# Kernel tuning notes

Hardware: AMD Instinct MI355X
Metric: run time of the kernel (lower is better)

Reference implementation:

```python
import jax, jax.numpy as jnp
import numpy as np

_SAMPLING_EPS = 1e-5
NEG_INF = jnp.float32(-jnp.inf)


def setup_inputs() -> dict:
    key = jax.random.key(0)
    k1, k2, k3, k4, k5 = jax.random.split(key, 5)
    B, V = 128, 128000
    logits = jax.random.normal(k1, (B, V), dtype=jnp.float32) * 4.0
    # every 8th row is greedy (temperature 0), rest random in [0.1, 1.5)
    rand_t = 0.1 + 1.4 * jax.random.uniform(k2, (B,), dtype=jnp.float32)
    temperatures = jnp.where(jnp.arange(B) % 8 == 0, 0.0, rand_t)
    top_k = jax.random.randint(k3, (B,), 1, 1001, dtype=jnp.int64)
    top_p = 0.1 + 0.9 * jax.random.uniform(k4, (B,), dtype=jnp.float32)
    # q ~ Exponential(1), replaces torch's generator-based q.exponential_()
    exp_noise = jax.random.exponential(k5, (B, V), dtype=jnp.float32)
    return {"logits": logits, "temperatures": temperatures, "top_k": top_k,
            "top_p": top_p, "exp_noise": exp_noise}


def _masked_logits(logits, temperatures, top_k, top_p):
    B, V = logits.shape
    # apply_temperature: greedy rows (temp < eps) divide by 1.0
    temp = jnp.where(temperatures < _SAMPLING_EPS, 1.0, temperatures)
    x = logits / temp[:, None]                       # [B, V]
    # ascending sort (as in torch code)
    sort_idx = jnp.argsort(x, axis=-1)               # [B, V]
    x_sort = jnp.take_along_axis(x, sort_idx, axis=-1)
    # top-k: keep the k largest (last k of ascending sort)
    k = jnp.clip(top_k, None, V).astype(jnp.int32)
    thr_idx = (V - k)[:, None]                       # [B, 1]
    thr = jnp.take_along_axis(x_sort, thr_idx, axis=-1)
    x_sort = jnp.where(x_sort < thr, NEG_INF, x_sort)
    # top-p on the sorted (ascending) logits
    probs_sort = jax.nn.softmax(x_sort, axis=-1)
    probs_sum = jnp.cumsum(probs_sort, axis=-1)
    p_mask = probs_sum <= (1.0 - top_p)[:, None]
    p_mask = p_mask.at[:, -1].set(False)             # always keep the max
    x_sort = jnp.where(p_mask, NEG_INF, x_sort)
    # scatter back to original positions: out[b, sort_idx[b, j]] = x_sort[b, j]
    rows = jnp.arange(B)[:, None]
    return x.at[rows, sort_idx].set(x_sort)


def reference(logits, temperatures, top_k, top_p, exp_noise):
    logits = logits.astype(jnp.float32)
    greedy = jnp.argmax(logits, axis=-1)             # [B]
    masked = _masked_logits(logits, temperatures, top_k, top_p)
    probs = jax.nn.softmax(masked, axis=-1)
    # Gumbel-max / exponential-race sampling: argmax(probs / q)
    random_sampled = jnp.argmax(probs / exp_noise, axis=-1)
    sampled = jnp.where(temperatures < _SAMPLING_EPS, greedy, random_sampled)
    return sampled[:, None].astype(jnp.int32)        # SamplerOutput.sampled_token_ids
```

## Files before the change

kernel.cpp:

```cpp
#include <hip/hip_runtime.h>
#include <stdint.h>

#define HB 4096
#define CAP 4096
#define SL1 20
#define SL3 20
#define THR1 256
#define THR4 1024
#define SEPS 1e-5f
#define ZMAX 8
#define LBUF 2048

typedef unsigned long long ull;

__device__ __forceinline__ uint32_t f2key(float x) {
  uint32_t u = __float_as_uint(x);
  return u ^ ((u & 0x80000000u) ? 0xFFFFFFFFu : 0x80000000u);
}
__device__ __forceinline__ float key2f(uint32_t k) {
  uint32_t u = (k & 0x80000000u) ? (k ^ 0x80000000u) : ~k;
  return __uint_as_float(u);
}

__global__ void k1_hist(const float* __restrict__ logits, const float* __restrict__ temps,
                        unsigned int* __restrict__ hist, ull* __restrict__ rowmax,
                        int V, int slice_len) {
  __shared__ unsigned int h[HB];
  __shared__ ull s_w64[THR1 / 64];
  int tid = threadIdx.x;
  int row = blockIdx.x / SL1;
  int slice = blockIdx.x % SL1;
  float tr = temps[row];
  int col_base = slice * slice_len;
  const float4* p4 = reinterpret_cast<const float4*>(logits + (size_t)row * V + col_base);
  int n4 = slice_len >> 2;

  if (tr < SEPS) {
    ull best = 0ULL;
    for (int v = tid; v < n4; v += THR1) {
      float4 f = p4[v];
      int c0 = col_base + 4 * v;
      float xs[4] = {f.x, f.y, f.z, f.w};
#pragma unroll
      for (int m = 0; m < 4; ++m) {
        ull pk = ((ull)f2key(xs[m]) << 32) | (ull)(uint32_t)(V - 1 - (c0 + m));
        if (pk > best) best = pk;
      }
    }
    for (int off = 32; off > 0; off >>= 1) {
      ull o = __shfl_down(best, off);
      if (o > best) best = o;
    }
    int lane = tid & 63, wid = tid >> 6;
    if (lane == 0) s_w64[wid] = best;
    __syncthreads();
    if (tid == 0) {
      ull b2 = s_w64[0];
      for (int w = 1; w < THR1 / 64; ++w) if (s_w64[w] > b2) b2 = s_w64[w];
      atomicMax(&rowmax[row], b2);
    }
    return;
  }

  for (int b = tid; b < HB; b += THR1) h[b] = 0;
  __syncthreads();
  for (int v = tid; v < n4; v += THR1) {
    float4 f = p4[v];
    float xs[4] = {f.x, f.y, f.z, f.w};
#pragma unroll
    for (int m = 0; m < 4; ++m) {
      uint32_t key = f2key(xs[m]);
      if (key >= 0x80000000u)
        atomicAdd(&h[(key & 0x7FFFFFFFu) >> 19], 1u);
    }
  }
  __syncthreads();
  for (int b = tid; b < HB; b += THR1) {
    unsigned int c = h[b];
    if (c) atomicAdd(&hist[(size_t)row * HB + b], c);
  }
}

__global__ void k2_select(const unsigned int* __restrict__ hist, const int* __restrict__ topk32,
                          unsigned int* __restrict__ tcap, int* __restrict__ kks, int B, int V) {
  __shared__ int s_flag;
  __shared__ unsigned int s_scan[256];
  int tid = threadIdx.x, row = blockIdx.x;
  if (tid == 0) { s_flag = 0; tcap[row] = 0x80000000u; }
  __syncthreads();
  if (tid < B && topk32[tid] == 0) s_flag = 1;
  __syncthreads();
  int kraw = s_flag ? topk32[2 * row] : topk32[row];
  int kk = kraw < 1 ? 1 : (kraw > V ? V : kraw);
  if (tid == 0) kks[row] = kk;
  unsigned int h[16];
  unsigned int csum = 0;
  const unsigned int* hr = hist + (size_t)row * HB;
#pragma unroll
  for (int c = 0; c < 16; ++c) { h[c] = hr[tid * 16 + c]; csum += h[c]; }
  s_scan[tid] = csum;
  __syncthreads();
  for (int off = 1; off < 256; off <<= 1) {
    unsigned int v = s_scan[tid];
    unsigned int u = (tid + off < 256) ? s_scan[tid + off] : 0u;
    __syncthreads();
    s_scan[tid] = v + u;
    __syncthreads();
  }
  unsigned int run = (tid < 255) ? s_scan[tid + 1] : 0u;
  for (int c = 15; c >= 0; --c) {
    unsigned int prev = run;
    run += h[c];
    if (run >= (unsigned int)kk && prev < (unsigned int)kk)
      tcap[row] = 0x80000000u | ((unsigned int)(tid * 16 + c) << 19);
  }
}

__global__ void k3_capture(const float* __restrict__ logits, const float* __restrict__ noise,
                           const float* __restrict__ temps, const unsigned int* __restrict__ tcap,
                           ull* __restrict__ cand, unsigned int* __restrict__ cnt,
                           unsigned int* __restrict__ zcnt, int* __restrict__ zlist,
                           int V, int slice_len) {
  __shared__ ull s_buf[LBUF];
  __shared__ unsigned int s_n, s_base;
  int tid = threadIdx.x;
  int row = blockIdx.x / SL3;
  int slice = blockIdx.x % SL3;
  if (temps[row] < SEPS) return;
  if (tid == 0) s_n = 0;
  __syncthreads();
  unsigned int tk = tcap[row];
  int col_base = slice * slice_len;
  const float4* p4 = reinterpret_cast<const float4*>(logits + (size_t)row * V + col_base);
  const float4* q4 = reinterpret_cast<const float4*>(noise + (size_t)row * V + col_base);
  int n4 = slice_len >> 2;
  for (int v = tid; v < n4; v += THR1) {
    float4 f = p4[v];
    float4 q = q4[v];
    int c0 = col_base + 4 * v;
    float xs[4] = {f.x, f.y, f.z, f.w};
    float qs[4] = {q.x, q.y, q.z, q.w};
#pragma unroll
    for (int m = 0; m < 4; ++m) {
      uint32_t key = f2key(xs[m]);
      if (key >= tk) {
        ull pk = ((ull)key << 32) | (ull)(uint32_t)(c0 + m);
        unsigned int pos = atomicAdd(&s_n, 1u);
        if (pos < LBUF) s_buf[pos] = pk;
        else {
          unsigned int g = atomicAdd(&cnt[row], 1u);
          if (g < CAP) cand[(size_t)row * CAP + g] = pk;
        }
      }
      if (qs[m] == 0.0f) {
        unsigned int p = atomicAdd(&zcnt[row], 1u);
        if (p < ZMAX) zlist[row * ZMAX + p] = c0 + m;
      }
    }
  }
  __syncthreads();
  unsigned int m = (s_n < LBUF) ? s_n : LBUF;
  if (tid == 0) s_base = atomicAdd(&cnt[row], m);
  __syncthreads();
  unsigned int base = s_base;
  for (unsigned int i = tid; i < m; i += THR1) {
    unsigned int g = base + i;
    if (g < CAP) cand[(size_t)row * CAP + g] = s_buf[i];
  }
}

__global__ __launch_bounds__(THR4) void k4_final(
    const ull* __restrict__ cand, const unsigned int* __restrict__ cnt,
    const int* __restrict__ kks, const float* __restrict__ temps,
    const float* __restrict__ topp, const float* __restrict__ noise,
    const ull* __restrict__ rowmax, const unsigned int* __restrict__ zcnt,
    const int* __restrict__ zlist, int* __restrict__ out, int V) {
  __shared__ ull s_cand[CAP];
  __shared__ float s_e[CAP];
  __shared__ unsigned char s_kept[CAP];
  __shared__ float s_w[16];
  __shared__ ull s_w64[16];
  __shared__ int s_nan, s_pz;
  int tid = threadIdx.x, row = blockIdx.x;
  int lane = tid & 63, wid = tid >> 6;
  float tr = temps[row];
  if (tr < SEPS) {
    if (tid == 0) {
      ull rm = rowmax[row];
      out[row] = V - 1 - (int)(uint32_t)(rm & 0xFFFFFFFFu);
    }
    return;
  }
  if (tid == 0) s_nan = 0x7FFFFFFF;
  unsigned int cv = cnt[row];
  int n = (cv < (unsigned int)CAP) ? (int)cv : CAP;
  if (n < 1) n = 1;
  int N = 64;
  while (N < n) N <<= 1;
  for (int i = tid; i < N; i += THR4) {
    ull pk = 0ULL;
    if (i < n) {
      ull c = cand[(size_t)row * CAP + i];
      float x = key2f((uint32_t)(c >> 32)) / tr;
      pk = ((ull)f2key(x) << 32) | (c & 0xFFFFFFFFu);
    }
    s_cand[i] = pk;
  }
  __syncthreads();
  for (int k = 2; k <= 64; k <<= 1) {
    for (int j = k >> 1; j > 0; j >>= 1) {
      for (int i = tid; i < N; i += THR4) {
        int l = i ^ j;
        if (l > i) {
          ull a = s_cand[i], b = s_cand[l];
          bool up = ((i & k) == 0);
          if (up ? (a < b) : (a > b)) { s_cand[i] = b; s_cand[l] = a; }
        }
      }
      __builtin_amdgcn_wave_barrier();
    }
  }
  __syncthreads();
  for (int k = 128; k <= N; k <<= 1) {
    for (int j = k >> 1; j >= 64; j >>= 1) {
      for (int i = tid; i < N; i += THR4) {
        int l = i ^ j;
        if (l > i) {
          ull a = s_cand[i], b = s_cand[l];
          bool up = ((i & k) == 0);
          if (up ? (a < b) : (a > b)) { s_cand[i] = b; s_cand[l] = a; }
        }
      }
      __syncthreads();
    }
    for (int j = 32; j > 0; j >>= 1) {
      for (int i = tid; i < N; i += THR4) {
        int l = i ^ j;
        if (l > i) {
          ull a = s_cand[i], b = s_cand[l];
          bool up = ((i & k) == 0);
          if (up ? (a < b) : (a > b)) { s_cand[i] = b; s_cand[l] = a; }
        }
      }
      __builtin_amdgcn_wave_barrier();
    }
    __syncthreads();
  }
  int kk = kks[row];
  if (kk > n) kk = n;
  uint32_t thrkey = (uint32_t)(s_cand[kk - 1] >> 32);
  float xmax = key2f((uint32_t)(s_cand[0] >> 32));
  int C = N / THR4;
  if (C < 1) C = 1;
  int i0 = tid * C;
  float csum = 0.f;
  for (int c = 0; c < C; ++c) {
    int i = i0 + c;
    if (i < N) {
      uint32_t key = (uint32_t)(s_cand[i] >> 32);
      float e = 0.f;
      if (i < n && key >= thrkey) e = expf(key2f(key) - xmax);
      s_e[i] = e;
      csum += e;
    }
  }
  {
    float v = csum;
    for (int off = 32; off > 0; off >>= 1) v += __shfl_xor(v, off);
    if (lane == 0) s_w[wid] = v;
  }
  __syncthreads();
  float Z1 = 0.f;
  for (int w = 0; w < 16; ++w) Z1 += s_w[w];
  float pcsum = 0.f;
  for (int c = 0; c < C; ++c) {
    int i = i0 + c;
    if (i < N) pcsum += s_e[i] / Z1;
  }
  float sfx = pcsum;
  for (int off = 1; off < 64; off <<= 1) {
    float o = __shfl_down(sfx, off);
    if (lane + off < 64) sfx += o;
  }
  __syncthreads();
  if (lane == 0) s_w[wid] = sfx;
  __syncthreads();
  float above = sfx - pcsum;
  for (int w = wid + 1; w < 16; ++w) above += s_w[w];
  float thresh = 1.0f - topp[row];
  float run = above, z2 = 0.f;
  for (int c = C - 1; c >= 0; --c) {
    int i = i0 + c;
    if (i < N) {
      run += s_e[i] / Z1;
      uint32_t key = (uint32_t)(s_cand[i] >> 32);
      bool kept = (i < n) && (key >= thrkey) && (run > thresh || i == 0);
      s_kept[i] = kept ? 1 : 0;
      if (kept) z2 += s_e[i];
    }
  }
  {
    float v = z2;
    for (int off = 32; off > 0; off >>= 1) v += __shfl_xor(v, off);
    __syncthreads();
    if (lane == 0) s_w[wid] = v;
  }
  __syncthreads();
  float Z2 = 0.f;
  for (int w = 0; w < 16; ++w) Z2 += s_w[w];
  unsigned int nzc = zcnt[row];
  int nz = (nzc < (unsigned int)ZMAX) ? (int)nzc : ZMAX;
  for (int zi = 0; zi < nz; ++zi) {
    int z = zlist[row * ZMAX + zi];
    if (tid == 0) s_pz = 0;
    __syncthreads();
    for (int c = 0; c < C; ++c) {
      int i = i0 + c;
      if (i < n && (int)(uint32_t)(s_cand[i] & 0xFFFFFFFFu) == z && s_kept[i] && s_e[i] > 0.f)
        s_pz = 1;
    }
    __syncthreads();
    if (tid == 0 && s_pz == 0 && z < s_nan) s_nan = z;
    __syncthreads();
  }
  const float* qrow = noise + (size_t)row * V;
  ull pk = 0ULL;
  for (int c = 0; c < C; ++c) {
    int i = i0 + c;
    if (i < N && s_kept[i]) {
      int idx = (int)(uint32_t)(s_cand[i] & 0xFFFFFFFFu);
      float r = (s_e[i] / Z2) / qrow[idx];
      ull p = ((ull)__float_as_uint(r) << 32) |
              (ull)(0xFFFFFFFFu - (uint32_t)idx);
      if (p > pk) pk = p;
    }
  }
  for (int off = 32; off > 0; off >>= 1) {
    ull o = __shfl_xor(pk, off);
    if (o > pk) pk = o;
  }
  if (lane == 0) s_w64[wid] = pk;
  __syncthreads();
  if (tid == 0) {
    ull best = s_w64[0];
    for (int w = 1; w < 16; ++w) if (s_w64[w] > best) best = s_w64[w];
    int winner = (int)(0xFFFFFFFFu - (uint32_t)(best & 0xFFFFFFFFu));
    if (s_nan != 0x7FFFFFFF) winner = s_nan;
    out[row] = winner;
  }
}

extern "C" void kernel_launch(void* const* d_in, const int* in_sizes, int n_in,
                              void* d_out, int out_size, void* d_ws, size_t ws_size,
                              hipStream_t stream) {
  const float* logits = (const float*)d_in[0];
  const float* temps  = (const float*)d_in[1];
  const int*   topk   = (const int*)d_in[2];
  const float* topp   = (const float*)d_in[3];
  const float* noise  = (const float*)d_in[4];
  int B = in_sizes[1];
  int V = in_sizes[0] / B;
  int slice1 = V / SL1;
  int slice3 = V / SL3;

  char* ws = (char*)d_ws;
  size_t off = 0;
  ull* cand = (ull*)(ws + off); off += (size_t)B * CAP * 8;
  size_t zstart = off;
  ull* rowmax = (ull*)(ws + off); off += (size_t)B * 8;
  unsigned int* hist = (unsigned int*)(ws + off); off += (size_t)B * HB * 4;
  unsigned int* tcap = (unsigned int*)(ws + off); off += (size_t)B * 4;
  int* kks = (int*)(ws + off); off += (size_t)B * 4;
  unsigned int* cnt = (unsigned int*)(ws + off); off += (size_t)B * 4;
  unsigned int* zcnt = (unsigned int*)(ws + off); off += (size_t)B * 4;
  size_t zend = off;
  int* zlist = (int*)(ws + off); off += (size_t)B * ZMAX * 4;

  hipMemsetAsync(ws + zstart, 0, zend - zstart, stream);
  k1_hist<<<dim3(B * SL1), dim3(THR1), 0, stream>>>(logits, temps, hist, rowmax, V, slice1);
  k2_select<<<dim3(B), dim3(256), 0, stream>>>(hist, topk, tcap, kks, B, V);
  k3_capture<<<dim3(B * SL3), dim3(THR1), 0, stream>>>(logits, noise, temps, tcap, cand, cnt,
                                                       zcnt, zlist, V, slice3);
  k4_final<<<dim3(B), dim3(THR4), 0, stream>>>(cand, cnt, kks, temps, topp, noise, rowmax,
                                               zcnt, zlist, (int*)d_out, V);
}
```

Measured before the change: 200.8 us.

## Fuse threshold selection into histogram kernel via last-block-done pattern

Merges the k2 select kernel into k1 using a per-row completion counter, so the last slice block of each row scans the global histogram and sets the top-k threshold. This removes one kernel launch. The zero-noise scan moves from the capture pass into the histogram pass. The histogram doubles to 8192 bins so the cut is finer and fewer candidates pass it, and the final kernel gathers noise into shared memory once. In exchange, k1 now reads the noise tensor, the workspace grows, and the scheme relies on threadfence and atomic-counter ordering being correct.

```diff
diff --git a/kernel.cpp b/kernel.cpp
--- a/kernel.cpp
+++ b/kernel.cpp
@@ -1,7 +1,8 @@
 #include <hip/hip_runtime.h>
 #include <stdint.h>
 
-#define HB 4096
+#define HB 8192
+#define HSH 18
 #define CAP 4096
 #define SL1 20
 #define SL3 20
@@ -22,11 +23,16 @@
   return __uint_as_float(u);
 }
 
-__global__ void k1_hist(const float* __restrict__ logits, const float* __restrict__ temps,
+__global__ void k1_hist(const float* __restrict__ logits, const float* __restrict__ noise,
+                        const float* __restrict__ temps, const int* __restrict__ topk32,
                         unsigned int* __restrict__ hist, ull* __restrict__ rowmax,
-                        int V, int slice_len) {
+                        unsigned int* __restrict__ zcnt, int* __restrict__ zlist,
+                        unsigned int* __restrict__ tcap, int* __restrict__ kks,
+                        unsigned int* __restrict__ done, int B, int V, int slice_len) {
   __shared__ unsigned int h[HB];
   __shared__ ull s_w64[THR1 / 64];
+  __shared__ unsigned int s_old;
+  __shared__ int s_flag;
   int tid = threadIdx.x;
   int row = blockIdx.x / SL1;
   int slice = blockIdx.x % SL1;
@@ -64,14 +70,22 @@
 
   for (int b = tid; b < HB; b += THR1) h[b] = 0;
   __syncthreads();
+  const float4* q4 = reinterpret_cast<const float4*>(noise + (size_t)row * V + col_base);
   for (int v = tid; v < n4; v += THR1) {
     float4 f = p4[v];
+    float4 q = q4[v];
+    int c0 = col_base + 4 * v;
     float xs[4] = {f.x, f.y, f.z, f.w};
+    float qs[4] = {q.x, q.y, q.z, q.w};
 #pragma unroll
     for (int m = 0; m < 4; ++m) {
       uint32_t key = f2key(xs[m]);
       if (key >= 0x80000000u)
-        atomicAdd(&h[(key & 0x7FFFFFFFu) >> 19], 1u);
+        atomicAdd(&h[(key & 0x7FFFFFFFu) >> HSH], 1u);
+      if (qs[m] == 0.0f) {
+        unsigned int p = atomicAdd(&zcnt[row], 1u);
+        if (p < ZMAX) zlist[row * ZMAX + p] = c0 + m;
+      }
     }
   }
   __syncthreads();
@@ -79,27 +93,26 @@
     unsigned int c = h[b];
     if (c) atomicAdd(&hist[(size_t)row * HB + b], c);
   }
-}
-
-__global__ void k2_select(const unsigned int* __restrict__ hist, const int* __restrict__ topk32,
-                          unsigned int* __restrict__ tcap, int* __restrict__ kks, int B, int V) {
-  __shared__ int s_flag;
-  __shared__ unsigned int s_scan[256];
-  int tid = threadIdx.x, row = blockIdx.x;
+  __threadfence();
+  if (tid == 0) s_old = atomicAdd(&done[row], 1u);
+  __syncthreads();
+  if (s_old != SL1 - 1) return;
+  __threadfence();
+
   if (tid == 0) { s_flag = 0; tcap[row] = 0x80000000u; }
   __syncthreads();
   if (tid < B && topk32[tid] == 0) s_flag = 1;
+  unsigned int hh[HB / 256];
+  unsigned int csum = 0;
+  const volatile unsigned int* hr = hist + (size_t)row * HB;
+#pragma unroll
+  for (int c = 0; c < HB / 256; ++c) { hh[c] = hr[tid * (HB / 256) + c]; csum += hh[c]; }
+  unsigned int* s_scan = h;
+  s_scan[tid] = csum;
   __syncthreads();
   int kraw = s_flag ? topk32[2 * row] : topk32[row];
   int kk = kraw < 1 ? 1 : (kraw > V ? V : kraw);
-  if (tid == 0) kks[row] = kk;
-  unsigned int h[16];
-  unsigned int csum = 0;
-  const unsigned int* hr = hist + (size_t)row * HB;
-#pragma unroll
-  for (int c = 0; c < 16; ++c) { h[c] = hr[tid * 16 + c]; csum += h[c]; }
-  s_scan[tid] = csum;
-  __syncthreads();
+  kks[row] = kk;
   for (int off = 1; off < 256; off <<= 1) {
     unsigned int v = s_scan[tid];
     unsigned int u = (tid + off < 256) ? s_scan[tid + off] : 0u;
@@ -108,18 +121,17 @@
     __syncthreads();
   }
   unsigned int run = (tid < 255) ? s_scan[tid + 1] : 0u;
-  for (int c = 15; c >= 0; --c) {
+  for (int c = HB / 256 - 1; c >= 0; --c) {
     unsigned int prev = run;
-    run += h[c];
+    run += hh[c];
     if (run >= (unsigned int)kk && prev < (unsigned int)kk)
-      tcap[row] = 0x80000000u | ((unsigned int)(tid * 16 + c) << 19);
-  }
-}
-
-__global__ void k3_capture(const float* __restrict__ logits, const float* __restrict__ noise,
-                           const float* __restrict__ temps, const unsigned int* __restrict__ tcap,
+      tcap[row] = 0x80000000u | ((unsigned int)(tid * (HB / 256) + c) << HSH);
+  }
+}
+
+__global__ void k3_capture(const float* __restrict__ logits, const float* __restrict__ temps,
+                           const unsigned int* __restrict__ tcap,
                            ull* __restrict__ cand, unsigned int* __restrict__ cnt,
-                           unsigned int* __restrict__ zcnt, int* __restrict__ zlist,
                            int V, int slice_len) {
   __shared__ ull s_buf[LBUF];
   __shared__ unsigned int s_n, s_base;
@@ -132,14 +144,11 @@
   unsigned int tk = tcap[row];
   int col_base = slice * slice_len;
   const float4* p4 = reinterpret_cast<const float4*>(logits + (size_t)row * V + col_base);
-  const float4* q4 = reinterpret_cast<const float4*>(noise + (size_t)row * V + col_base);
   int n4 = slice_len >> 2;
   for (int v = tid; v < n4; v += THR1) {
     float4 f = p4[v];
-    float4 q = q4[v];
     int c0 = col_base + 4 * v;
     float xs[4] = {f.x, f.y, f.z, f.w};
-    float qs[4] = {q.x, q.y, q.z, q.w};
 #pragma unroll
     for (int m = 0; m < 4; ++m) {
       uint32_t key = f2key(xs[m]);
@@ -152,10 +161,6 @@
           if (g < CAP) cand[(size_t)row * CAP + g] = pk;
         }
       }
-      if (qs[m] == 0.0f) {
-        unsigned int p = atomicAdd(&zcnt[row], 1u);
-        if (p < ZMAX) zlist[row * ZMAX + p] = c0 + m;
-      }
     }
   }
   __syncthreads();
@@ -177,6 +182,7 @@
     const int* __restrict__ zlist, int* __restrict__ out, int V) {
   __shared__ ull s_cand[CAP];
   __shared__ float s_e[CAP];
+  __shared__ float s_q[CAP];
   __shared__ unsigned char s_kept[CAP];
   __shared__ float s_w[16];
   __shared__ ull s_w64[16];
@@ -253,11 +259,14 @@
   int C = N / THR4;
   if (C < 1) C = 1;
   int i0 = tid * C;
+  const float* qrow = noise + (size_t)row * V;
   float csum = 0.f;
   for (int c = 0; c < C; ++c) {
     int i = i0 + c;
     if (i < N) {
-      uint32_t key = (uint32_t)(s_cand[i] >> 32);
+      ull cd = s_cand[i];
+      uint32_t key = (uint32_t)(cd >> 32);
+      if (i < n) s_q[i] = qrow[(uint32_t)(cd & 0xFFFFFFFFu)];
       float e = 0.f;
       if (i < n && key >= thrkey) e = expf(key2f(key) - xmax);
       s_e[i] = e;
@@ -323,13 +332,12 @@
     if (tid == 0 && s_pz == 0 && z < s_nan) s_nan = z;
     __syncthreads();
   }
-  const float* qrow = noise + (size_t)row * V;
   ull pk = 0ULL;
   for (int c = 0; c < C; ++c) {
     int i = i0 + c;
     if (i < N && s_kept[i]) {
       int idx = (int)(uint32_t)(s_cand[i] & 0xFFFFFFFFu);
-      float r = (s_e[i] / Z2) / qrow[idx];
+      float r = (s_e[i] / Z2) / s_q[i];
       ull p = ((ull)__float_as_uint(r) << 32) |
               (ull)(0xFFFFFFFFu - (uint32_t)idx);
       if (p > pk) pk = p;
@@ -373,14 +381,14 @@
   int* kks = (int*)(ws + off); off += (size_t)B * 4;
   unsigned int* cnt = (unsigned int*)(ws + off); off += (size_t)B * 4;
   unsigned int* zcnt = (unsigned int*)(ws + off); off += (size_t)B * 4;
+  unsigned int* done = (unsigned int*)(ws + off); off += (size_t)B * 4;
   size_t zend = off;
   int* zlist = (int*)(ws + off); off += (size_t)B * ZMAX * 4;
 
   hipMemsetAsync(ws + zstart, 0, zend - zstart, stream);
-  k1_hist<<<dim3(B * SL1), dim3(THR1), 0, stream>>>(logits, temps, hist, rowmax, V, slice1);
-  k2_select<<<dim3(B), dim3(256), 0, stream>>>(hist, topk, tcap, kks, B, V);
-  k3_capture<<<dim3(B * SL3), dim3(THR1), 0, stream>>>(logits, noise, temps, tcap, cand, cnt,
-                                                       zcnt, zlist, V, slice3);
+  k1_hist<<<dim3(B * SL1), dim3(THR1), 0, stream>>>(logits, noise, temps, topk, hist, rowmax,
+                                                    zcnt, zlist, tcap, kks, done, B, V, slice1);
+  k3_capture<<<dim3(B * SL3), dim3(THR1), 0, stream>>>(logits, temps, tcap, cand, cnt, V, slice3);
   k4_final<<<dim3(B), dim3(THR4), 0, stream>>>(cand, cnt, kks, temps, topp, noise, rowmax,
                                                zcnt, zlist, (int*)d_out, V);
 }
```

Result: slower. 537.3 us (+167.6%).
